# Kernel tuning notes

Measured on AMD Instinct MI355X. Metric: run time of the kernel, lower is better.

Reference implementation:

```python
import jax, jax.numpy as jnp
import numpy as np

BLOCK_N = 64  # KV tile size used by the Triton kernel (affects numerics: kernel is not exact softmax)


def _flash_fwd_buggy(q, k, v, sm_scale):
    """Faithful reproduction of the kernel's online-softmax loop.

    Note: the original kernel omits the accumulator rescaling step of true
    flash attention (acc is accumulated with the *running* denominator and
    never corrected), so we replicate that block-wise update exactly.
    q: [B,H,Sq,D], k/v: [B,H,Sk,D], Sk % BLOCK_N == 0.
    """
    B, H, Sq, D = q.shape
    Sk = k.shape[2]
    nblk = Sk // BLOCK_N
    # [nblk, B, H, BLOCK_N, D]
    kb = jnp.moveaxis(k.reshape(B, H, nblk, BLOCK_N, D), 2, 0)
    vb = jnp.moveaxis(v.reshape(B, H, nblk, BLOCK_N, D), 2, 0)

    acc0 = jnp.zeros((B, H, Sq, D), dtype=jnp.float32)
    m0 = jnp.full((B, H, Sq), -jnp.inf, dtype=jnp.float32)
    l0 = jnp.zeros((B, H, Sq), dtype=jnp.float32)

    def step(carry, kv):
        acc, m_prev, l_prev = carry
        kblk, vblk = kv  # [B,H,BLOCK_N,D]
        qk = jnp.einsum('bhmd,bhnd->bhmn', q, kblk) * sm_scale  # [B,H,Sq,BLOCK_N]
        m_curr = jnp.maximum(jnp.max(qk, axis=-1), m_prev)
        qk_exp = jnp.exp(qk - m_curr[..., None])
        l_curr = jnp.sum(qk_exp, axis=-1)
        l_new = l_prev * jnp.exp(m_prev - m_curr) + l_curr
        p = qk_exp / l_new[..., None]
        acc = acc + jnp.einsum('bhmn,bhnd->bhmd', p, vblk)
        return (acc, m_curr, l_new), None

    (acc, _, _), _ = jax.lax.scan(step, (acc0, m0, l0), (kb, vb))
    return acc


def setup_inputs() -> dict:
    key = jax.random.key(0)
    kq, kk, kv = jax.random.split(key, 3)
    B, H, S, D = 2, 16, 4096, 128
    q = jax.random.normal(kq, (B, H, S, D), dtype=jnp.float32)
    k = jax.random.normal(kk, (B, H, S, D), dtype=jnp.float32)
    v = jax.random.normal(kv, (B, H, S, D), dtype=jnp.float32)
    return {"q": q, "k": k, "v": v}


def reference(q, k, v):
    head_dim = q.shape[-1]
    sm_scale = 1.0 / np.sqrt(head_dim).astype(np.float32)
    # causal=False, dropout=0.0 (module defaults); module returns (output, None)
    return _flash_fwd_buggy(q, k, v, sm_scale)
```

## Files before the change

kernel.cpp:

```cpp
#include <hip/hip_runtime.h>
#include <hip/hip_bf16.h>
#include <math.h>


typedef __attribute__((ext_vector_type(8)))  unsigned short ushort8;
typedef __attribute__((ext_vector_type(8)))  __bf16        bf16x8;
typedef __attribute__((ext_vector_type(16))) float         f32x16;
typedef __attribute__((ext_vector_type(4)))  float         floatv4;
typedef __attribute__((ext_vector_type(2)))  unsigned int  uint2v;
typedef __attribute__((ext_vector_type(4)))  unsigned int  uint4v;

#define SQ   4096
#define SKV  4096
#define DH   128
#define BN   64
#define QB   256
#define NT   (SKV / BN)
#define KLD  136
#define VTLD 72
#define KBUF (64 * KLD)
#define VBUF (DH * VTLD)

static __device__ __forceinline__ unsigned pk2(float lo, float hi) {
    unsigned r;
    asm("v_cvt_pk_bf16_f32 %0, %1, %2" : "=v"(r) : "v"(lo), "v"(hi));
    return r;
}

__global__ __launch_bounds__(512, 2) void fa_fwd_buggy(
    const float* __restrict__ Qg, const float* __restrict__ Kg,
    const float* __restrict__ Vg, float* __restrict__ Og)
{
    __shared__ unsigned short K_lds[2 * KBUF];
    __shared__ unsigned short Vt_lds[3 * VBUF];

    const int tid  = threadIdx.x;
    const int w    = tid >> 6;
    const int lane = tid & 63;
    const int c32  = lane & 31;
    const int h    = lane >> 5;

    const int wgid  = blockIdx.x;
    const int bh    = (wgid & 7) * 4 + (wgid >> 7);
    const int qtile = (wgid >> 3) & 15;
    const int qbase = qtile * QB;
    const float qscale = 0.08838834764831845f * 1.44269504088896341f;

    const float* Qrow = Qg + ((size_t)bh * SQ + qbase + w * 32 + c32) * DH;
    ushort8 qf[8];
    #pragma unroll
    for (int ds = 0; ds < 8; ++ds) {
        floatv4 a = *(const floatv4*)(Qrow + ds * 16 + h * 8);
        floatv4 b = *(const floatv4*)(Qrow + ds * 16 + h * 8 + 4);
        uint4v u;
        u[0] = pk2(a[0]*qscale, a[1]*qscale);
        u[1] = pk2(a[2]*qscale, a[3]*qscale);
        u[2] = pk2(b[0]*qscale, b[1]*qscale);
        u[3] = pk2(b[2]*qscale, b[3]*qscale);
        qf[ds] = __builtin_bit_cast(ushort8, u);
    }

    f32x16 acc[4];
    #pragma unroll
    for (int i = 0; i < 4; ++i)
        #pragma unroll
        for (int r = 0; r < 16; ++r) acc[i][r] = 0.f;

    float l_run = 0.f;

    const float* Kbh = Kg + (size_t)bh * SKV * DH;
    const float* Vbh = Vg + (size_t)bh * SKV * DH;

    const int n_k = tid >> 3;
    const int u_k = tid & 7;
    const int dq  = tid & 31;
    const int nq  = tid >> 5;
    const int vswz = (dq >> 1) & 7;

    floatv4 ka0, ka1, kb0, kb1;
    floatv4 va0, va1, va2, va3;

#define LOAD_TILE(N0) do {                                                   \
        const float* ks_ = Kbh + (size_t)((N0) + n_k) * DH + u_k * 8;        \
        ka0 = *(const floatv4*)(ks_);        ka1 = *(const floatv4*)(ks_+4); \
        kb0 = *(const floatv4*)(ks_ + 64);   kb1 = *(const floatv4*)(ks_+68);\
        const float* vs_ = Vbh + (size_t)((N0) + nq * 4) * DH + dq * 4;      \
        va0 = *(const floatv4*)(vs_);        va1 = *(const floatv4*)(vs_+DH);\
        va2 = *(const floatv4*)(vs_+2*DH);   va3 = *(const floatv4*)(vs_+3*DH);\
    } while (0)

#define STORE_TILE(KS, VS) do {                                              \
        unsigned short* kd_ = &K_lds[(KS) * KBUF];                           \
        unsigned short* vd_ = &Vt_lds[(VS) * VBUF];                          \
        uint4v u_;                                                           \
        u_[0]=pk2(ka0[0],ka0[1]); u_[1]=pk2(ka0[2],ka0[3]);                  \
        u_[2]=pk2(ka1[0],ka1[1]); u_[3]=pk2(ka1[2],ka1[3]);                  \
        *(uint4v*)&kd_[n_k * KLD + u_k * 8] = u_;                            \
        u_[0]=pk2(kb0[0],kb0[1]); u_[1]=pk2(kb0[2],kb0[3]);                  \
        u_[2]=pk2(kb1[0],kb1[1]); u_[3]=pk2(kb1[2],kb1[3]);                  \
        *(uint4v*)&kd_[n_k * KLD + (u_k + 8) * 8] = u_;                      \
        _Pragma("unroll")                                                    \
        for (int i_ = 0; i_ < 4; ++i_) {                                     \
            const int d_ = dq * 4 + i_;                                      \
            uint2v p_;                                                       \
            p_[0] = pk2(va0[i_], va1[i_]);                                   \
            p_[1] = pk2(va2[i_], va3[i_]);                                   \
            const int unit_ = (nq >> 1) ^ vswz;                              \
            *(uint2v*)&vd_[d_ * VTLD + unit_ * 8 + (nq & 1) * 4] = p_;       \
        }                                                                    \
    } while (0)

#define QK_TILE(S0, S1, KS) do {                                             \
        const unsigned short* kb_ = &K_lds[(KS) * KBUF];                     \
        f32x16 t0_, t1_;                                                     \
        _Pragma("unroll")                                                    \
        for (int r_ = 0; r_ < 16; ++r_) { t0_[r_] = 0.f; t1_[r_] = 0.f; }    \
        __builtin_amdgcn_s_setprio(1);                                       \
        _Pragma("unroll")                                                    \
        for (int ds_ = 0; ds_ < 8; ++ds_) {                                  \
            ushort8 kf0_ = *(const ushort8*)&kb_[(c32)      * KLD + ds_*16 + h*8]; \
            ushort8 kf1_ = *(const ushort8*)&kb_[(32 + c32) * KLD + ds_*16 + h*8]; \
            t0_ = __builtin_amdgcn_mfma_f32_32x32x16_bf16(                   \
                    __builtin_bit_cast(bf16x8, kf0_),                        \
                    __builtin_bit_cast(bf16x8, qf[ds_]), t0_, 0, 0, 0);      \
            t1_ = __builtin_amdgcn_mfma_f32_32x32x16_bf16(                   \
                    __builtin_bit_cast(bf16x8, kf1_),                        \
                    __builtin_bit_cast(bf16x8, qf[ds_]), t1_, 0, 0, 0);      \
        }                                                                    \
        __builtin_amdgcn_s_setprio(0);                                       \
        S0 = t0_; S1 = t1_;                                                  \
    } while (0)

#define SM_PACK(S0, S1, PA) do {                                             \
        float ps_ = 0.f;                                                     \
        _Pragma("unroll")                                                    \
        for (int r_ = 0; r_ < 16; ++r_) S0[r_] = __builtin_amdgcn_exp2f(S0[r_]); \
        _Pragma("unroll")                                                    \
        for (int r_ = 0; r_ < 16; ++r_) S1[r_] = __builtin_amdgcn_exp2f(S1[r_]); \
        {                                                                    \
            float q0_ = (S0[0]+S0[1])+(S0[2]+S0[3]);                         \
            float q1_ = (S0[4]+S0[5])+(S0[6]+S0[7]);                         \
            float q2_ = (S0[8]+S0[9])+(S0[10]+S0[11]);                       \
            float q3_ = (S0[12]+S0[13])+(S0[14]+S0[15]);                     \
            float q4_ = (S1[0]+S1[1])+(S1[2]+S1[3]);                         \
            float q5_ = (S1[4]+S1[5])+(S1[6]+S1[7]);                         \
            float q6_ = (S1[8]+S1[9])+(S1[10]+S1[11]);                       \
            float q7_ = (S1[12]+S1[13])+(S1[14]+S1[15]);                     \
            ps_ = ((q0_+q1_)+(q2_+q3_)) + ((q4_+q5_)+(q6_+q7_));             \
        }                                                                    \
        ps_ += __shfl_xor(ps_, 32);                                          \
        const float ln_ = l_run + ps_;                                       \
        l_run = ln_;                                                         \
        const float inv_ = __builtin_amdgcn_rcpf(ln_);                       \
        unsigned wrd_[2][8];                                                 \
        _Pragma("unroll")                                                    \
        for (int i_ = 0; i_ < 8; ++i_)                                       \
            wrd_[0][i_] = pk2(S0[2*i_] * inv_, S0[2*i_+1] * inv_);           \
        _Pragma("unroll")                                                    \
        for (int i_ = 0; i_ < 8; ++i_)                                       \
            wrd_[1][i_] = pk2(S1[2*i_] * inv_, S1[2*i_+1] * inv_);           \
        _Pragma("unroll")                                                    \
        for (int st_ = 0; st_ < 4; ++st_) {                                  \
            const int ns_   = st_ >> 1;                                      \
            const int base_ = 4 * (st_ & 1);                                 \
            auto rA_ = __builtin_amdgcn_permlane32_swap(                     \
                          (int)wrd_[ns_][base_ + 0], (int)wrd_[ns_][base_ + 2], false, false); \
            auto rB_ = __builtin_amdgcn_permlane32_swap(                     \
                          (int)wrd_[ns_][base_ + 1], (int)wrd_[ns_][base_ + 3], false, false); \
            uint4v pw_;                                                      \
            pw_[0] = (unsigned)rA_[0];                                       \
            pw_[1] = (unsigned)rB_[0];                                       \
            pw_[2] = (unsigned)rA_[1];                                       \
            pw_[3] = (unsigned)rB_[1];                                       \
            PA[st_] = __builtin_bit_cast(ushort8, pw_);                      \
        }                                                                    \
    } while (0)

#define PV_TILE(PA, VS) do {                                                 \
        const unsigned short* vb_ = &Vt_lds[(VS) * VBUF];                    \
        __builtin_amdgcn_s_setprio(1);                                       \
        _Pragma("unroll")                                                    \
        for (int dt_ = 0; dt_ < 4; ++dt_) {                                  \
            const int d_  = dt_ * 32 + c32;                                  \
            const int fz_ = (d_ >> 3) & 7;                                   \
            _Pragma("unroll")                                                \
            for (int st_ = 0; st_ < 4; ++st_) {                              \
                ushort8 vv_ = *(const ushort8*)&vb_[d_ * VTLD + (((2*st_ + h) ^ fz_) * 8)]; \
                acc[dt_] = __builtin_amdgcn_mfma_f32_32x32x16_bf16(          \
                    __builtin_bit_cast(bf16x8, PA[st_]),                     \
                    __builtin_bit_cast(bf16x8, vv_), acc[dt_], 0, 0, 0);     \
            }                                                                \
        }                                                                    \
        __builtin_amdgcn_s_setprio(0);                                       \
    } while (0)

    LOAD_TILE(0);
    STORE_TILE(0, 0);
    LOAD_TILE(BN);
    __syncthreads();

    f32x16 sA0, sA1, sB0, sB1;
    QK_TILE(sA0, sA1, 0);

    int vs0 = 0;
    for (int t = 0; t < NT; t += 2) {
        const int vs1 = (vs0 == 2) ? 0 : vs0 + 1;
        const int vs2 = (vs1 == 2) ? 0 : vs1 + 1;

        STORE_TILE(1, vs1);
        if (t + 2 < NT) LOAD_TILE((size_t)(t + 2) * BN);
        __syncthreads();
        QK_TILE(sB0, sB1, 1);
        {
            ushort8 pa[4];
            SM_PACK(sA0, sA1, pa);
            PV_TILE(pa, vs0);
        }

        if (t + 2 < NT) {
            STORE_TILE(0, vs2);
            if (t + 3 < NT) LOAD_TILE((size_t)(t + 3) * BN);
        }
        __syncthreads();
        if (t + 2 < NT) QK_TILE(sA0, sA1, 0);
        {
            ushort8 pa[4];
            SM_PACK(sB0, sB1, pa);
            PV_TILE(pa, vs1);
        }

        vs0 = vs2;
    }

    float* ob = Og + ((size_t)bh * SQ + qbase + w * 32) * DH + c32;
    #pragma unroll
    for (int dt = 0; dt < 4; ++dt) {
        #pragma unroll
        for (int r = 0; r < 16; ++r) {
            const int qrow = (r & 3) + 8 * (r >> 2) + 4 * h;
            ob[(size_t)qrow * DH + dt * 32] = acc[dt][r];
        }
    }
}

extern "C" void kernel_launch(void* const* d_in, const int* in_sizes, int n_in,
                              void* d_out, int out_size, void* d_ws, size_t ws_size,
                              hipStream_t stream) {
    const float* q = (const float*)d_in[0];
    const float* k = (const float*)d_in[1];
    const float* v = (const float*)d_in[2];
    float* o = (float*)d_out;
    dim3 grid((SQ / QB) * 32);
    fa_fwd_buggy<<<grid, 512, 0, stream>>>(q, k, v, o);
}
```

Baseline: 296.6 us.

## Replace software-pipelined QK/PV schedule with per-tile body and double-buffered V

Drops the cross-iteration pipeline in which QK of the next tile overlapped softmax/PV of the current one, along with the triple-buffered V. Each tile now runs QK on its first 32-key half, stores and prefetches the next tile between the two QK halves, then does softmax and PV, with one barrier per tile. This lowers LDS use (V goes from three buffers to two) and register pressure from holding two S tiles live. The cost is less MFMA/exp overlap across tiles, since QK and PV are now serialized within each tile.

```diff
diff --git a/kernel.cpp b/kernel.cpp
--- a/kernel.cpp
+++ b/kernel.cpp
@@ -32,7 +32,7 @@
     const float* __restrict__ Vg, float* __restrict__ Og)
 {
     __shared__ unsigned short K_lds[2 * KBUF];
-    __shared__ unsigned short Vt_lds[3 * VBUF];
+    __shared__ unsigned short Vt_lds[2 * VBUF];
 
     const int tid  = threadIdx.x;
     const int w    = tid >> 6;
@@ -89,9 +89,9 @@
         va2 = *(const floatv4*)(vs_+2*DH);   va3 = *(const floatv4*)(vs_+3*DH);\
     } while (0)
 
-#define STORE_TILE(KS, VS) do {                                              \
-        unsigned short* kd_ = &K_lds[(KS) * KBUF];                           \
-        unsigned short* vd_ = &Vt_lds[(VS) * VBUF];                          \
+#define STORE_TILE(B) do {                                                   \
+        unsigned short* kd_ = &K_lds[(B) * KBUF];                            \
+        unsigned short* vd_ = &Vt_lds[(B) * VBUF];                           \
         uint4v u_;                                                           \
         u_[0]=pk2(ka0[0],ka0[1]); u_[1]=pk2(ka0[2],ka0[3]);                  \
         u_[2]=pk2(ka1[0],ka1[1]); u_[3]=pk2(ka1[2],ka1[3]);                  \
@@ -110,44 +110,44 @@
         }                                                                    \
     } while (0)
 
-#define QK_TILE(S0, S1, KS) do {                                             \
-        const unsigned short* kb_ = &K_lds[(KS) * KBUF];                     \
-        f32x16 t0_, t1_;                                                     \
-        _Pragma("unroll")                                                    \
-        for (int r_ = 0; r_ < 16; ++r_) { t0_[r_] = 0.f; t1_[r_] = 0.f; }    \
+#define QK_NS(S, BUF, NS) do {                                               \
+        const unsigned short* kb_ = &K_lds[(BUF) * KBUF];                    \
+        _Pragma("unroll")                                                    \
+        for (int r_ = 0; r_ < 16; ++r_) S[r_] = 0.f;                         \
         __builtin_amdgcn_s_setprio(1);                                       \
         _Pragma("unroll")                                                    \
         for (int ds_ = 0; ds_ < 8; ++ds_) {                                  \
-            ushort8 kf0_ = *(const ushort8*)&kb_[(c32)      * KLD + ds_*16 + h*8]; \
-            ushort8 kf1_ = *(const ushort8*)&kb_[(32 + c32) * KLD + ds_*16 + h*8]; \
-            t0_ = __builtin_amdgcn_mfma_f32_32x32x16_bf16(                   \
-                    __builtin_bit_cast(bf16x8, kf0_),                        \
-                    __builtin_bit_cast(bf16x8, qf[ds_]), t0_, 0, 0, 0);      \
-            t1_ = __builtin_amdgcn_mfma_f32_32x32x16_bf16(                   \
-                    __builtin_bit_cast(bf16x8, kf1_),                        \
-                    __builtin_bit_cast(bf16x8, qf[ds_]), t1_, 0, 0, 0);      \
+            ushort8 kf_ = *(const ushort8*)&kb_[((NS) * 32 + c32) * KLD      \
+                                                + ds_ * 16 + h * 8];         \
+            S = __builtin_amdgcn_mfma_f32_32x32x16_bf16(                     \
+                    __builtin_bit_cast(bf16x8, kf_),                         \
+                    __builtin_bit_cast(bf16x8, qf[ds_]), S, 0, 0, 0);        \
         }                                                                    \
         __builtin_amdgcn_s_setprio(0);                                       \
-        S0 = t0_; S1 = t1_;                                                  \
-    } while (0)
-
-#define SM_PACK(S0, S1, PA) do {                                             \
-        float ps_ = 0.f;                                                     \
-        _Pragma("unroll")                                                    \
-        for (int r_ = 0; r_ < 16; ++r_) S0[r_] = __builtin_amdgcn_exp2f(S0[r_]); \
-        _Pragma("unroll")                                                    \
-        for (int r_ = 0; r_ < 16; ++r_) S1[r_] = __builtin_amdgcn_exp2f(S1[r_]); \
-        {                                                                    \
-            float q0_ = (S0[0]+S0[1])+(S0[2]+S0[3]);                         \
-            float q1_ = (S0[4]+S0[5])+(S0[6]+S0[7]);                         \
-            float q2_ = (S0[8]+S0[9])+(S0[10]+S0[11]);                       \
-            float q3_ = (S0[12]+S0[13])+(S0[14]+S0[15]);                     \
-            float q4_ = (S1[0]+S1[1])+(S1[2]+S1[3]);                         \
-            float q5_ = (S1[4]+S1[5])+(S1[6]+S1[7]);                         \
-            float q6_ = (S1[8]+S1[9])+(S1[10]+S1[11]);                       \
-            float q7_ = (S1[12]+S1[13])+(S1[14]+S1[15]);                     \
-            ps_ = ((q0_+q1_)+(q2_+q3_)) + ((q4_+q5_)+(q6_+q7_));             \
-        }                                                                    \
+    } while (0)
+
+#define TILE_BODY(T, BUF) do {                                               \
+        f32x16 s0, s1;                                                       \
+        QK_NS(s0, BUF, 0);                                                   \
+        if ((T) + 1 < NT) {                                                  \
+            STORE_TILE(1 - (BUF));                                           \
+            if ((T) + 2 < NT) LOAD_TILE((size_t)((T) + 2) * BN);             \
+        }                                                                    \
+        QK_NS(s1, BUF, 1);                                                   \
+                                      \
+        _Pragma("unroll")                                                    \
+        for (int r_ = 0; r_ < 16; ++r_) s0[r_] = __builtin_amdgcn_exp2f(s0[r_]); \
+        _Pragma("unroll")                                                    \
+        for (int r_ = 0; r_ < 16; ++r_) s1[r_] = __builtin_amdgcn_exp2f(s1[r_]); \
+        float q0_ = (s0[0]+s0[1])+(s0[2]+s0[3]);                             \
+        float q1_ = (s0[4]+s0[5])+(s0[6]+s0[7]);                             \
+        float q2_ = (s0[8]+s0[9])+(s0[10]+s0[11]);                           \
+        float q3_ = (s0[12]+s0[13])+(s0[14]+s0[15]);                         \
+        float q4_ = (s1[0]+s1[1])+(s1[2]+s1[3]);                             \
+        float q5_ = (s1[4]+s1[5])+(s1[6]+s1[7]);                             \
+        float q6_ = (s1[8]+s1[9])+(s1[10]+s1[11]);                           \
+        float q7_ = (s1[12]+s1[13])+(s1[14]+s1[15]);                         \
+        float ps_ = ((q0_+q1_)+(q2_+q3_)) + ((q4_+q5_)+(q6_+q7_));           \
         ps_ += __shfl_xor(ps_, 32);                                          \
         const float ln_ = l_run + ps_;                                       \
         l_run = ln_;                                                         \
@@ -155,29 +155,27 @@
         unsigned wrd_[2][8];                                                 \
         _Pragma("unroll")                                                    \
         for (int i_ = 0; i_ < 8; ++i_)                                       \
-            wrd_[0][i_] = pk2(S0[2*i_] * inv_, S0[2*i_+1] * inv_);           \
+            wrd_[0][i_] = pk2(s0[2*i_] * inv_, s0[2*i_+1] * inv_);           \
         _Pragma("unroll")                                                    \
         for (int i_ = 0; i_ < 8; ++i_)                                       \
-            wrd_[1][i_] = pk2(S1[2*i_] * inv_, S1[2*i_+1] * inv_);           \
+            wrd_[1][i_] = pk2(s1[2*i_] * inv_, s1[2*i_+1] * inv_);           \
+        ushort8 pa_[4];                                                      \
         _Pragma("unroll")                                                    \
         for (int st_ = 0; st_ < 4; ++st_) {                                  \
             const int ns_   = st_ >> 1;                                      \
             const int base_ = 4 * (st_ & 1);                                 \
             auto rA_ = __builtin_amdgcn_permlane32_swap(                     \
-                          (int)wrd_[ns_][base_ + 0], (int)wrd_[ns_][base_ + 2], false, false); \
+                (int)wrd_[ns_][base_ + 0], (int)wrd_[ns_][base_ + 2], false, false); \
             auto rB_ = __builtin_amdgcn_permlane32_swap(                     \
-                          (int)wrd_[ns_][base_ + 1], (int)wrd_[ns_][base_ + 3], false, false); \
+                (int)wrd_[ns_][base_ + 1], (int)wrd_[ns_][base_ + 3], false, false); \
             uint4v pw_;                                                      \
             pw_[0] = (unsigned)rA_[0];                                       \
             pw_[1] = (unsigned)rB_[0];                                       \
             pw_[2] = (unsigned)rA_[1];                                       \
             pw_[3] = (unsigned)rB_[1];                                       \
-            PA[st_] = __builtin_bit_cast(ushort8, pw_);                      \
-        }                                                                    \
-    } while (0)
-
-#define PV_TILE(PA, VS) do {                                                 \
-        const unsigned short* vb_ = &Vt_lds[(VS) * VBUF];                    \
+            pa_[st_] = __builtin_bit_cast(ushort8, pw_);                     \
+        }                                                                    \
+        const unsigned short* vb_ = &Vt_lds[(BUF) * VBUF];                   \
         __builtin_amdgcn_s_setprio(1);                                       \
         _Pragma("unroll")                                                    \
         for (int dt_ = 0; dt_ < 4; ++dt_) {                                  \
@@ -185,51 +183,25 @@
             const int fz_ = (d_ >> 3) & 7;                                   \
             _Pragma("unroll")                                                \
             for (int st_ = 0; st_ < 4; ++st_) {                              \
-                ushort8 vv_ = *(const ushort8*)&vb_[d_ * VTLD + (((2*st_ + h) ^ fz_) * 8)]; \
+                ushort8 vv_ = *(const ushort8*)&vb_[d_ * VTLD                \
+                                  + (((2*st_ + h) ^ fz_) * 8)];              \
                 acc[dt_] = __builtin_amdgcn_mfma_f32_32x32x16_bf16(          \
-                    __builtin_bit_cast(bf16x8, PA[st_]),                     \
+                    __builtin_bit_cast(bf16x8, pa_[st_]),                    \
                     __builtin_bit_cast(bf16x8, vv_), acc[dt_], 0, 0, 0);     \
             }                                                                \
         }                                                                    \
         __builtin_amdgcn_s_setprio(0);                                       \
+        __syncthreads();                                                     \
     } while (0)
 
     LOAD_TILE(0);
-    STORE_TILE(0, 0);
+    STORE_TILE(0);
     LOAD_TILE(BN);
     __syncthreads();
 
-    f32x16 sA0, sA1, sB0, sB1;
-    QK_TILE(sA0, sA1, 0);
-
-    int vs0 = 0;
     for (int t = 0; t < NT; t += 2) {
-        const int vs1 = (vs0 == 2) ? 0 : vs0 + 1;
-        const int vs2 = (vs1 == 2) ? 0 : vs1 + 1;
-
-        STORE_TILE(1, vs1);
-        if (t + 2 < NT) LOAD_TILE((size_t)(t + 2) * BN);
-        __syncthreads();
-        QK_TILE(sB0, sB1, 1);
-        {
-            ushort8 pa[4];
-            SM_PACK(sA0, sA1, pa);
-            PV_TILE(pa, vs0);
-        }
-
-        if (t + 2 < NT) {
-            STORE_TILE(0, vs2);
-            if (t + 3 < NT) LOAD_TILE((size_t)(t + 3) * BN);
-        }
-        __syncthreads();
-        if (t + 2 < NT) QK_TILE(sA0, sA1, 0);
-        {
-            ushort8 pa[4];
-            SM_PACK(sB0, sB1, pa);
-            PV_TILE(pa, vs1);
-        }
-
-        vs0 = vs2;
+        TILE_BODY(t,     0);
+        TILE_BODY(t + 1, 1);
     }
 
     float* ob = Og + ((size_t)bh * SQ + qbase + w * 32) * DH + c32;
```

After: 290.7 us. -2.0%, faster.
